# Kernel tuning notes

Measured on AMD Instinct MI355X. Metric: run time of the kernel, lower is better.

## Reference

```python
import jax, jax.numpy as jnp
import numpy as np
from jax import lax

KS, STRIDE, DIL, PAD = 3, 1, 1, 1
B, C_IN, C_OUT, D = 1, 16, 16, 64
K = KS ** 3


def setup_inputs():
    key = jax.random.key(0)
    k1, k2, k3 = jax.random.split(key, 3)
    x = jax.random.normal(k1, (B, C_IN, D, D, D), jnp.float32)
    std = 1.0 / float(np.sqrt(C_IN * K))
    kernel = jax.random.uniform(k2, (K, C_IN, C_OUT), jnp.float32, -std, std)
    # module zero-inits pkernel; use small random values so interp path is exercised
    pkernel = jax.random.normal(k3, (K, C_IN, 3 * K), jnp.float32) * 0.01
    return {"x": x, "kernel": kernel, "pkernel": pkernel}


def _deform_conv3d(x, kernel, pkernel):
    Bn, C, Dd, H, W = x.shape
    Kt = kernel.shape[0]
    # offset-predicting conv: pkernel [K, C_in, 3K] -> conv weight [3K, C_in, kd, kh, kw]
    w_off = jnp.transpose(pkernel.reshape(KS, KS, KS, C, 3 * Kt), (4, 3, 0, 1, 2))
    off = lax.conv_general_dilated(
        x, w_off, (STRIDE,) * 3, [(PAD, PAD)] * 3,
        rhs_dilation=(DIL,) * 3,
        dimension_numbers=("NCDHW", "OIDHW", "NCDHW"))
    Do, Ho, Wo = off.shape[2], off.shape[3], off.shape[4]
    off = off.reshape(Bn, Kt, 3, Do, Ho, Wo)  # 3 offset coords per kernel tap

    # base sampling grid: out_pos*stride - pad + tap*dilation, then add predicted offset
    r = jnp.arange(KS)
    tap = jnp.stack(jnp.meshgrid(r, r, r, indexing="ij"), -1).reshape(Kt, 3) * DIL - PAD
    gz = (jnp.arange(Do) * STRIDE).astype(x.dtype)
    gy = (jnp.arange(Ho) * STRIDE).astype(x.dtype)
    gx = (jnp.arange(Wo) * STRIDE).astype(x.dtype)
    cz = gz[None, None, :, None, None] + tap[None, :, 0, None, None, None] + off[:, :, 0]
    cy = gy[None, None, None, :, None] + tap[None, :, 1, None, None, None] + off[:, :, 1]
    cx = gx[None, None, None, None, :] + tap[None, :, 2, None, None, None] + off[:, :, 2]

    x_flat = x.reshape(Bn, C, Dd * H * W)

    def gather(idx):  # idx [B,K,Do,Ho,Wo] int32 -> [B,C,K,Do,Ho,Wo]
        g = jax.vmap(lambda xf, ix: xf[:, ix.reshape(-1)])(x_flat, idx)
        return g.reshape(Bn, C, Kt, Do, Ho, Wo)

    z0f = jnp.floor(cz); y0f = jnp.floor(cy); x0f = jnp.floor(cx)
    fz, fy, fx = cz - z0f, cy - y0f, cx - x0f
    z0 = z0f.astype(jnp.int32); y0 = y0f.astype(jnp.int32); x0 = x0f.astype(jnp.int32)

    # trilinear interp: accumulate 8 corners (zero outside volume)
    acc = jnp.zeros((Bn, C, Kt, Do, Ho, Wo), x.dtype)
    for dz in (0, 1):
        for dy in (0, 1):
            for dx in (0, 1):
                zi, yi, xi = z0 + dz, y0 + dy, x0 + dx
                valid = ((zi >= 0) & (zi < Dd) & (yi >= 0) & (yi < H)
                         & (xi >= 0) & (xi < W)).astype(x.dtype)
                w = ((fz if dz else 1.0 - fz) * (fy if dy else 1.0 - fy)
                     * (fx if dx else 1.0 - fx)) * valid
                idx = (jnp.clip(zi, 0, Dd - 1) * (H * W)
                       + jnp.clip(yi, 0, H - 1) * W + jnp.clip(xi, 0, W - 1))
                acc = acc + gather(idx) * w[:, None]

    # weighted sum over taps: kernel [K, C_in, C_out]
    return jnp.einsum("bckdhw,kco->bodhw", acc, kernel)


def reference(x, kernel, pkernel):
    return _deform_conv3d(x, kernel, pkernel)
```

## Files before the change

kernel.cpp:

```cpp
#include <hip/hip_runtime.h>

#define D 64
#define DD 4096
#define DDD 262144
#define K 27

typedef _Float16 half8  __attribute__((ext_vector_type(8)));
typedef _Float16 half2v __attribute__((ext_vector_type(2)));
typedef float    f32x4  __attribute__((ext_vector_type(4)));
typedef float    f32x2  __attribute__((ext_vector_type(2)));

__device__ inline half2v pk2(float w) {
    return __builtin_bit_cast(half2v, __builtin_amdgcn_cvt_pkrtz(w, w));
}

#define HX 12
#define HY 8
#define HZ 6
#define HROW 12
#define HPLN 96
#define HSP  576
#define CPAD 16
#define OSTR 72

#define WSW_CH (14*6*64)
#define KSW_CH (14*64)
#define KSW_OFF 86016

__device__ inline half2v h2of(half8 v, int d) {
    half2v r; r.x = v[2*d]; r.y = v[2*d+1]; return r;
}

__global__ __launch_bounds__(256) void prep_weights(const float* __restrict__ pk,
                                                    const float* __restrict__ kern,
                                                    _Float16* __restrict__ Wsw,
                                                    _Float16* __restrict__ Ksw) {
    int t = blockIdx.x * 256 + threadIdx.x;
    if (t < WSW_CH) {
        int lane = t & 63;
        int sm = t >> 6;
        int s = sm / 6, mt = sm - 6 * s;
        int m = mt * 16 + (lane & 15);
        int q = lane >> 4;
        half8 w;
#pragma unroll
        for (int j = 0; j < 8; ++j) {
            int k = 32 * s + 8 * q + j;
            int kt = k >> 4, c = k & 15;
            float wv = (kt < K && m < 81) ? pk[kt * 1296 + c * 81 + m] : 0.0f;
            w[j] = (_Float16)wv;
        }
        *(half8*)(Wsw + t * 8) = w;
    } else if (t < WSW_CH + KSW_CH) {
        int u = t - WSW_CH;
        int s = u >> 6, lane = u & 63;
        int o = lane & 15, q = lane >> 4;
        half8 w;
#pragma unroll
        for (int j = 0; j < 8; ++j) {
            int k = q * 8 + j;
            int kt = 2 * s + (k >> 4), c = k & 15;
            float wv = (kt < K) ? kern[kt * 256 + c * 16 + o] : 0.0f;
            w[j] = (_Float16)wv;
        }
        *(half8*)(Ksw + u * 8) = w;
    }
}

__global__ __launch_bounds__(256, 5) void deform_main(
    const float* __restrict__ x,
    const _Float16* __restrict__ Wsw,
    const _Float16* __restrict__ Ksw,
    float* __restrict__ out)
{
    __shared__ _Float16 s_h[HSP * CPAD];
    __shared__ _Float16 s_off[81 * OSTR];

    const int tid  = threadIdx.x;
    const int lane = tid & 63;
    const int wave = __builtin_amdgcn_readfirstlane(tid >> 6);

    const int bx0 = blockIdx.x * 8;
    const int by0 = blockIdx.y * 4;
    const int bz0 = blockIdx.z * 2;

    for (int i = tid; i < HSP; i += 256) {
        int z = i / HPLN;
        int r = i - z * HPLN;
        int y = r / HROW;
        int xx = r - y * HROW;
        int gz = bz0 - 2 + z, gy = by0 - 2 + y, gx = bx0 - 2 + xx;
        bool in = (unsigned)gz < D && (unsigned)gy < D && (unsigned)gx < D;
        half8 a = {}, b = {};
        if (in) {
            const float* p = x + (gz * DD + gy * D + gx);
#pragma unroll
            for (int c = 0; c < 8; ++c) a[c] = (_Float16)p[c * DDD];
#pragma unroll
            for (int c = 0; c < 8; ++c) b[c] = (_Float16)p[(c + 8) * DDD];
        }
        *(half8*)(s_h + i * CPAD)     = a;
        *(half8*)(s_h + i * CPAD + 8) = b;
    }
    __syncthreads();

    const int n = lane & 15, q = lane >> 4;
    const int tz = wave >> 1;
    const int ty = 2 * (wave & 1) + (n >> 3);
    const int tx = n & 7;
    const int v = wave * 16 + n;

    {
        f32x4 acc[6] = {};
        for (int s = 0; s < 14; ++s) {
            int kt = 2 * s + (q >> 1);
            int ktc = (kt < K) ? kt : 0;
            int kd = ktc / 9, kh = (ktc / 3) % 3, kw = ktc % 3;
            int idx = (tz + kd + 1) * HPLN + (ty + kh + 1) * HROW + (tx + kw + 1);
            half8 bfrag = *(const half8*)(s_h + idx * CPAD + (q & 1) * 8);
#pragma unroll
            for (int mt = 0; mt < 6; ++mt) {
                half8 afrag = *(const half8*)(Wsw + ((s * 6 + mt) * 64 + lane) * 8);
                acc[mt] = __builtin_amdgcn_mfma_f32_16x16x32_f16(afrag, bfrag, acc[mt], 0, 0, 0);
            }
        }
#pragma unroll
        for (int mt = 0; mt < 6; ++mt)
#pragma unroll
            for (int r = 0; r < 4; ++r) {
                int o = mt * 16 + q * 4 + r;
                if (o < 81) s_off[o * OSTR + v] = (_Float16)acc[mt][r];
            }
    }
    __syncthreads();

    const int gz = bz0 + tz, gy = by0 + ty, gx = bx0 + tx;
    const int cbase = (q & 1) * 8;
    const int qh = q >> 1;

    f32x4 acc2 = {};

#pragma unroll
    for (int s = 0; s < 14; ++s) {
        const int ktr = 2 * s + qh;
        const int kt = (ktr < K) ? ktr : K - 1;
        const int kd = kt / 9, kh = (kt / 3) % 3, kw = kt % 3;

        const _Float16* offp = s_off + (3 * kt) * OSTR + v;
        float cz = (float)(gz + kd - 1) + (float)offp[0];
        float cy = (float)(gy + kh - 1) + (float)offp[OSTR];
        float cx = (float)(gx + kw - 1) + (float)offp[2 * OSTR];
        float zf = floorf(cz), yf = floorf(cy), xf = floorf(cx);
        float fz = cz - zf, fy = cy - yf, fx = cx - xf;
        int z0 = (int)zf, y0 = (int)yf, x0 = (int)xf;
        int hz0 = z0 - bz0 + 2, hy0 = y0 - by0 + 2, hx0 = x0 - bx0 + 2;

        half2v val2[4] = {};
        if ((unsigned)hz0 < (unsigned)(HZ - 1) && (unsigned)hy0 < (unsigned)(HY - 1)
            && (unsigned)hx0 < (unsigned)(HX - 1)) {
            const _Float16* cp = s_h + (hz0 * HPLN + hy0 * HROW + hx0) * CPAD + cbase;
            float gz1 = 1.0f - fz, gy1 = 1.0f - fy, gx1 = 1.0f - fx;
            float wyx00 = gy1 * gx1, wyx01 = gy1 * fx;
            float wyx10 = fy * gx1,  wyx11 = fy * fx;
#pragma unroll
            for (int dz = 0; dz < 2; ++dz) {
                float wz = dz ? fz : gz1;
                const _Float16* cpz = cp + dz * (HPLN * CPAD);
                half2v h00 = pk2(wz * wyx00);
                half2v h01 = pk2(wz * wyx01);
                half2v h10 = pk2(wz * wyx10);
                half2v h11 = pk2(wz * wyx11);
                half8 c00 = *(const half8*)(cpz);
                half8 c01 = *(const half8*)(cpz + CPAD);
                half8 c10 = *(const half8*)(cpz + HROW * CPAD);
                half8 c11 = *(const half8*)(cpz + (HROW + 1) * CPAD);
#pragma unroll
                for (int d = 0; d < 4; ++d) {
                    val2[d] += h00 * h2of(c00, d);
                    val2[d] += h01 * h2of(c01, d);
                    val2[d] += h10 * h2of(c10, d);
                    val2[d] += h11 * h2of(c11, d);
                }
            }
        } else {
            f32x2 valf[4] = {};
#pragma unroll
            for (int dz = 0; dz < 2; ++dz) {
                int zi = z0 + dz;
                float wz = dz ? fz : 1.0f - fz;
#pragma unroll
                for (int dy = 0; dy < 2; ++dy) {
                    int yi = y0 + dy;
                    float wzy = wz * (dy ? fy : 1.0f - fy);
#pragma unroll
                    for (int dx = 0; dx < 2; ++dx) {
                        int xi = x0 + dx;
                        if ((unsigned)zi < D && (unsigned)yi < D && (unsigned)xi < D) {
                            float w = wzy * (dx ? fx : 1.0f - fx);
                            int base = zi * DD + yi * D + xi;
#pragma unroll
                            for (int d = 0; d < 4; ++d) {
                                valf[d].x += w * x[(cbase + 2 * d)     * DDD + base];
                                valf[d].y += w * x[(cbase + 2 * d + 1) * DDD + base];
                            }
                        }
                    }
                }
            }
#pragma unroll
            for (int d = 0; d < 4; ++d) {
                val2[d].x = (_Float16)valf[d].x;
                val2[d].y = (_Float16)valf[d].y;
            }
        }

        half8 bf;
#pragma unroll
        for (int d = 0; d < 4; ++d) { bf[2*d] = val2[d].x; bf[2*d+1] = val2[d].y; }
        half8 af = *(const half8*)(Ksw + (s * 64 + lane) * 8);
        acc2 = __builtin_amdgcn_mfma_f32_16x16x32_f16(af, bf, acc2, 0, 0, 0);
    }

    const int opos = gz * DD + gy * D + gx;
#pragma unroll
    for (int r = 0; r < 4; ++r) {
        int o = q * 4 + r;
        out[o * DDD + opos] = acc2[r];
    }
}

extern "C" void kernel_launch(void* const* d_in, const int* in_sizes, int n_in,
                              void* d_out, int out_size, void* d_ws, size_t ws_size,
                              hipStream_t stream) {
    const float* x    = (const float*)d_in[0];
    const float* kern = (const float*)d_in[1];
    const float* pk   = (const float*)d_in[2];
    float* out = (float*)d_out;

    _Float16* Wsw = (_Float16*)d_ws;
    _Float16* Ksw = (_Float16*)((char*)d_ws + KSW_OFF);

    prep_weights<<<25, 256, 0, stream>>>(pk, kern, Wsw, Ksw);
    deform_main<<<dim3(8, 16, 32), 256, 0, stream>>>(x, Wsw, Ksw, out);
}
```

Before: 150.6 us.

## Split halo channels into two planes and give each lane all 16 channels per tap

The shared halo tile moves from interleaved 16-channel records to two separate 8-channel planes. In the sampling stage each lane now handles one tap with all 16 channels, covering 4 taps per step over 7 steps, where before it handled 2 taps with 8 channels over 14 steps. This removes the duplicated per-lane coordinate, floor and weight computation that was repeated across channel halves. Tap base offsets are precomputed into a small workspace table, and the interpolation uses halo-local coordinates directly. The change raises register use per lane (double the accumulators and loads) and changes the LDS access pattern, which may hurt occupancy or introduce bank conflicts.

```diff
diff --git a/kernel.cpp b/kernel.cpp
--- a/kernel.cpp
+++ b/kernel.cpp
@@ -12,6 +12,9 @@
 
 __device__ inline half2v pk2(float w) {
     return __builtin_bit_cast(half2v, __builtin_amdgcn_cvt_pkrtz(w, w));
+}
+__device__ inline half2v h2of(half8 v, int d) {
+    half2v r; r.x = v[2*d]; r.y = v[2*d+1]; return r;
 }
 
 #define HX 12
@@ -20,21 +23,19 @@
 #define HROW 12
 #define HPLN 96
 #define HSP  576
-#define CPAD 16
+#define HSPH 4608
 #define OSTR 72
 
 #define WSW_CH (14*6*64)
 #define KSW_CH (14*64)
 #define KSW_OFF 86016
-
-__device__ inline half2v h2of(half8 v, int d) {
-    half2v r; r.x = v[2*d]; r.y = v[2*d+1]; return r;
-}
+#define TAPF_OFF (KSW_OFF + KSW_CH*16)
 
 __global__ __launch_bounds__(256) void prep_weights(const float* __restrict__ pk,
                                                     const float* __restrict__ kern,
                                                     _Float16* __restrict__ Wsw,
-                                                    _Float16* __restrict__ Ksw) {
+                                                    _Float16* __restrict__ Ksw,
+                                                    float* __restrict__ tapf) {
     int t = blockIdx.x * 256 + threadIdx.x;
     if (t < WSW_CH) {
         int lane = t & 63;
@@ -53,17 +54,28 @@
         *(half8*)(Wsw + t * 8) = w;
     } else if (t < WSW_CH + KSW_CH) {
         int u = t - WSW_CH;
-        int s = u >> 6, lane = u & 63;
-        int o = lane & 15, q = lane >> 4;
+        int lane = u & 63;
+        int cch = u >> 6;
+        int s = cch >> 1, h = cch & 1;
+        int o = lane & 15;
+        int tap = 4 * s + (lane >> 4);
         half8 w;
 #pragma unroll
         for (int j = 0; j < 8; ++j) {
-            int k = q * 8 + j;
-            int kt = 2 * s + (k >> 4), c = k & 15;
-            float wv = (kt < K) ? kern[kt * 256 + c * 16 + o] : 0.0f;
+            int ch = h * 8 + j;
+            float wv = (tap < K) ? kern[tap * 256 + ch * 16 + o] : 0.0f;
             w[j] = (_Float16)wv;
         }
         *(half8*)(Ksw + u * 8) = w;
+    } else if (t < WSW_CH + KSW_CH + 28) {
+        int kt = t - WSW_CH - KSW_CH;
+        int ktc = (kt < K) ? kt : K - 1;
+        f32x4 b;
+        b.x = (float)(ktc / 9 + 1);
+        b.y = (float)((ktc / 3) % 3 + 1);
+        b.z = (float)(ktc % 3 + 1);
+        b.w = 0.0f;
+        *(f32x4*)(tapf + kt * 4) = b;
     }
 }
 
@@ -71,9 +83,10 @@
     const float* __restrict__ x,
     const _Float16* __restrict__ Wsw,
     const _Float16* __restrict__ Ksw,
+    const float* __restrict__ tapf,
     float* __restrict__ out)
 {
-    __shared__ _Float16 s_h[HSP * CPAD];
+    __shared__ _Float16 s_h[2 * HSPH];
     __shared__ _Float16 s_off[81 * OSTR];
 
     const int tid  = threadIdx.x;
@@ -99,8 +112,8 @@
 #pragma unroll
             for (int c = 0; c < 8; ++c) b[c] = (_Float16)p[(c + 8) * DDD];
         }
-        *(half8*)(s_h + i * CPAD)     = a;
-        *(half8*)(s_h + i * CPAD + 8) = b;
+        *(half8*)(s_h + i * 8)        = a;
+        *(half8*)(s_h + HSPH + i * 8) = b;
     }
     __syncthreads();
 
@@ -117,7 +130,7 @@
             int ktc = (kt < K) ? kt : 0;
             int kd = ktc / 9, kh = (ktc / 3) % 3, kw = ktc % 3;
             int idx = (tz + kd + 1) * HPLN + (ty + kh + 1) * HROW + (tx + kw + 1);
-            half8 bfrag = *(const half8*)(s_h + idx * CPAD + (q & 1) * 8);
+            half8 bfrag = *(const half8*)(s_h + (q & 1) * HSPH + idx * 8);
 #pragma unroll
             for (int mt = 0; mt < 6; ++mt) {
                 half8 afrag = *(const half8*)(Wsw + ((s * 6 + mt) * 64 + lane) * 8);
@@ -134,56 +147,61 @@
     }
     __syncthreads();
 
-    const int gz = bz0 + tz, gy = by0 + ty, gx = bx0 + tx;
-    const int cbase = (q & 1) * 8;
-    const int qh = q >> 1;
-
+    const float bzf = (float)tz, byf = (float)ty, bxf = (float)tx;
     f32x4 acc2 = {};
 
 #pragma unroll
-    for (int s = 0; s < 14; ++s) {
-        const int ktr = 2 * s + qh;
+    for (int s = 0; s < 7; ++s) {
+        const int ktr = 4 * s + q;
         const int kt = (ktr < K) ? ktr : K - 1;
-        const int kd = kt / 9, kh = (kt / 3) % 3, kw = kt % 3;
-
+
+        const f32x4 tb = *(const f32x4*)(tapf + kt * 4);
         const _Float16* offp = s_off + (3 * kt) * OSTR + v;
-        float cz = (float)(gz + kd - 1) + (float)offp[0];
-        float cy = (float)(gy + kh - 1) + (float)offp[OSTR];
-        float cx = (float)(gx + kw - 1) + (float)offp[2 * OSTR];
-        float zf = floorf(cz), yf = floorf(cy), xf = floorf(cx);
-        float fz = cz - zf, fy = cy - yf, fx = cx - xf;
-        int z0 = (int)zf, y0 = (int)yf, x0 = (int)xf;
-        int hz0 = z0 - bz0 + 2, hy0 = y0 - by0 + 2, hx0 = x0 - bx0 + 2;
-
-        half2v val2[4] = {};
+        float lz = bzf + tb.x + (float)offp[0];
+        float ly = byf + tb.y + (float)offp[OSTR];
+        float lx = bxf + tb.z + (float)offp[2 * OSTR];
+        float zf = floorf(lz), yf = floorf(ly), xf = floorf(lx);
+        float fz = lz - zf, fy = ly - yf, fx = lx - xf;
+        int hz0 = (int)zf, hy0 = (int)yf, hx0 = (int)xf;
+
+        half2v val2[8] = {};
         if ((unsigned)hz0 < (unsigned)(HZ - 1) && (unsigned)hy0 < (unsigned)(HY - 1)
             && (unsigned)hx0 < (unsigned)(HX - 1)) {
-            const _Float16* cp = s_h + (hz0 * HPLN + hy0 * HROW + hx0) * CPAD + cbase;
+            const _Float16* cpl = s_h + (hz0 * HPLN + hy0 * HROW + hx0) * 8;
             float gz1 = 1.0f - fz, gy1 = 1.0f - fy, gx1 = 1.0f - fx;
             float wyx00 = gy1 * gx1, wyx01 = gy1 * fx;
             float wyx10 = fy * gx1,  wyx11 = fy * fx;
 #pragma unroll
             for (int dz = 0; dz < 2; ++dz) {
                 float wz = dz ? fz : gz1;
-                const _Float16* cpz = cp + dz * (HPLN * CPAD);
+                const _Float16* cz_ = cpl + dz * (HPLN * 8);
                 half2v h00 = pk2(wz * wyx00);
                 half2v h01 = pk2(wz * wyx01);
                 half2v h10 = pk2(wz * wyx10);
                 half2v h11 = pk2(wz * wyx11);
-                half8 c00 = *(const half8*)(cpz);
-                half8 c01 = *(const half8*)(cpz + CPAD);
-                half8 c10 = *(const half8*)(cpz + HROW * CPAD);
-                half8 c11 = *(const half8*)(cpz + (HROW + 1) * CPAD);
+                half8 l00 = *(const half8*)(cz_);
+                half8 l01 = *(const half8*)(cz_ + 8);
+                half8 l10 = *(const half8*)(cz_ + HROW * 8);
+                half8 l11 = *(const half8*)(cz_ + (HROW + 1) * 8);
+                half8 u00 = *(const half8*)(cz_ + HSPH);
+                half8 u01 = *(const half8*)(cz_ + HSPH + 8);
+                half8 u10 = *(const half8*)(cz_ + HSPH + HROW * 8);
+                half8 u11 = *(const half8*)(cz_ + HSPH + (HROW + 1) * 8);
 #pragma unroll
                 for (int d = 0; d < 4; ++d) {
-                    val2[d] += h00 * h2of(c00, d);
-                    val2[d] += h01 * h2of(c01, d);
-                    val2[d] += h10 * h2of(c10, d);
-                    val2[d] += h11 * h2of(c11, d);
+                    val2[d]     += h00 * h2of(l00, d);
+                    val2[d]     += h01 * h2of(l01, d);
+                    val2[d]     += h10 * h2of(l10, d);
+                    val2[d]     += h11 * h2of(l11, d);
+                    val2[4 + d] += h00 * h2of(u00, d);
+                    val2[4 + d] += h01 * h2of(u01, d);
+                    val2[4 + d] += h10 * h2of(u10, d);
+                    val2[4 + d] += h11 * h2of(u11, d);
                 }
             }
         } else {
-            f32x2 valf[4] = {};
+            int z0 = hz0 + bz0 - 2, y0 = hy0 + by0 - 2, x0 = hx0 + bx0 - 2;
+            f32x2 valf[8] = {};
 #pragma unroll
             for (int dz = 0; dz < 2; ++dz) {
                 int zi = z0 + dz;
@@ -199,28 +217,34 @@
                             float w = wzy * (dx ? fx : 1.0f - fx);
                             int base = zi * DD + yi * D + xi;
 #pragma unroll
-                            for (int d = 0; d < 4; ++d) {
-                                valf[d].x += w * x[(cbase + 2 * d)     * DDD + base];
-                                valf[d].y += w * x[(cbase + 2 * d + 1) * DDD + base];
+                            for (int d = 0; d < 8; ++d) {
+                                valf[d].x += w * x[(2 * d)     * DDD + base];
+                                valf[d].y += w * x[(2 * d + 1) * DDD + base];
                             }
                         }
                     }
                 }
             }
 #pragma unroll
-            for (int d = 0; d < 4; ++d) {
+            for (int d = 0; d < 8; ++d) {
                 val2[d].x = (_Float16)valf[d].x;
                 val2[d].y = (_Float16)valf[d].y;
             }
         }
 
-        half8 bf;
-#pragma unroll
-        for (int d = 0; d < 4; ++d) { bf[2*d] = val2[d].x; bf[2*d+1] = val2[d].y; }
-        half8 af = *(const half8*)(Ksw + (s * 64 + lane) * 8);
-        acc2 = __builtin_amdgcn_mfma_f32_16x16x32_f16(af, bf, acc2, 0, 0, 0);
-    }
-
+        half8 blo, bhi;
+#pragma unroll
+        for (int d = 0; d < 4; ++d) {
+            blo[2*d] = val2[d].x;     blo[2*d+1] = val2[d].y;
+            bhi[2*d] = val2[4+d].x;   bhi[2*d+1] = val2[4+d].y;
+        }
+        half8 alo = *(const half8*)(Ksw + ((2*s)     * 64 + lane) * 8);
+        half8 ahi = *(const half8*)(Ksw + ((2*s + 1) * 64 + lane) * 8);
+        acc2 = __builtin_amdgcn_mfma_f32_16x16x32_f16(alo, blo, acc2, 0, 0, 0);
+        acc2 = __builtin_amdgcn_mfma_f32_16x16x32_f16(ahi, bhi, acc2, 0, 0, 0);
+    }
+
+    const int gz = bz0 + tz, gy = by0 + ty, gx = bx0 + tx;
     const int opos = gz * DD + gy * D + gx;
 #pragma unroll
     for (int r = 0; r < 4; ++r) {
@@ -239,7 +263,8 @@
 
     _Float16* Wsw = (_Float16*)d_ws;
     _Float16* Ksw = (_Float16*)((char*)d_ws + KSW_OFF);
-
-    prep_weights<<<25, 256, 0, stream>>>(pk, kern, Wsw, Ksw);
-    deform_main<<<dim3(8, 16, 32), 256, 0, stream>>>(x, Wsw, Ksw, out);
-}
+    float* tapf   = (float*)((char*)d_ws + TAPF_OFF);
+
+    prep_weights<<<25, 256, 0, stream>>>(pk, kern, Wsw, Ksw, tapf);
+    deform_main<<<dim3(8, 16, 32), 256, 0, stream>>>(x, Wsw, Ksw, tapf, out);
+}
```

After: 147.2 us. 2.2% less time.
